# Optimization experiments

Hardware: AMD Instinct MI355X
Metric: run time of the kernel (lower is better)

The kernel has to match this reference:

```python
import jax, jax.numpy as jnp
import numpy as np

D_MODEL = 1024
HEADDIM = 64
EXPAND = 2
D_STATE = 128
D_CONV = 4
NGROUPS = 1
D_INNER = EXPAND * D_MODEL            # 2048
NHEADS = D_INNER // HEADDIM           # 32
CONV_DIM = D_INNER + 2 * NGROUPS * D_STATE
D_IN_PROJ = 2 * D_INNER + 2 * NGROUPS * D_STATE + NHEADS
BATCH = 2
SEQLEN = 1024
EPS = 1e-5


def silu(v):
    return v * jax.nn.sigmoid(v)


def setup_inputs() -> dict:
    key = jax.random.key(0)
    ks = jax.random.split(key, 8)
    s = 0.02
    return {
        "x": jax.random.normal(ks[0], (BATCH, SEQLEN, D_MODEL), jnp.float32),
        "in_proj_w": jax.random.normal(ks[1], (D_IN_PROJ, D_MODEL), jnp.float32) * s,
        "conv_w": jax.random.normal(ks[2], (CONV_DIM, D_CONV), jnp.float32) * 0.2,
        "conv_b": jax.random.normal(ks[3], (CONV_DIM,), jnp.float32) * 0.02,
        "dt_bias": jax.random.normal(ks[4], (NHEADS,), jnp.float32) * 0.1,
        "A_log": jax.random.normal(ks[5], (NHEADS,), jnp.float32) * 0.5,
        "D": jax.random.normal(ks[6], (NHEADS,), jnp.float32) * 0.5,
        "norm_w": jnp.ones((D_INNER,), jnp.float32),
        "out_proj_w": jax.random.normal(ks[7], (D_MODEL, D_INNER), jnp.float32) * s,
    }


def _mamba2(x, in_proj_w, conv_w, conv_b, dt_bias, A_log, D, norm_w, out_proj_w):
    b, l, _ = x.shape
    # input projection -> z | xBC | dt
    zxbcdt = x @ in_proj_w.T                                  # [b,l,d_in_proj]
    z, xBC, dt = jnp.split(zxbcdt, [D_INNER, D_INNER + CONV_DIM], axis=-1)
    dt = jax.nn.softplus(dt + dt_bias)                        # [b,l,nh]
    # causal depthwise conv over time, then SiLU
    rhs = conv_w.T[:, None, :]                                # [d_conv, 1, conv_dim]
    xBC = jax.lax.conv_general_dilated(
        xBC, rhs, window_strides=(1,), padding=[(D_CONV - 1, 0)],
        dimension_numbers=("NWC", "WIO", "NWC"), feature_group_count=CONV_DIM)
    xBC = silu(xBC + conv_b)
    xs, Bm, Cm = jnp.split(xBC, [D_INNER, D_INNER + D_STATE], axis=-1)
    xs = xs.reshape(b, l, NHEADS, HEADDIM)                    # [b,l,h,p]
    A = -jnp.exp(A_log)                                       # [nh], negative
    dA = jnp.exp(dt * A)                                      # [b,l,nh] in (0,1)
    # selective scan: h_t = dA_t * h_{t-1} + dt_t * x_t (outer) B_t; y_t = h_t C_t
    def step(h, inp):
        dA_t, x_t, B_t, dt_t, C_t = inp                       # [b,h],[b,h,p],[b,n],[b,h],[b,n]
        h = h * dA_t[:, :, None, None] + jnp.einsum("bh,bhp,bn->bhpn", dt_t, x_t, B_t)
        y = jnp.einsum("bhpn,bn->bhp", h, C_t)
        return h, y

    h0 = jnp.zeros((b, NHEADS, HEADDIM, D_STATE), x.dtype)
    xs_t = xs.transpose(1, 0, 2, 3)
    _, ys = jax.lax.scan(step, h0, (dA.transpose(1, 0, 2), xs_t,
                                    Bm.transpose(1, 0, 2), dt.transpose(1, 0, 2),
                                    Cm.transpose(1, 0, 2)))
    y = ys.transpose(1, 0, 2, 3) + D[None, None, :, None] * xs  # skip term
    y = y.reshape(b, l, D_INNER)
    # gated RMSNorm (norm_before_gate=False): rmsnorm(y * silu(z)) * w
    y = y * silu(z)
    y = y * jax.lax.rsqrt(jnp.mean(y * y, axis=-1, keepdims=True) + EPS) * norm_w
    return y @ out_proj_w.T


def reference(x, in_proj_w, conv_w, conv_b, dt_bias, A_log, D, norm_w, out_proj_w):
    return x + _mamba2(x, in_proj_w, conv_w, conv_b, dt_bias, A_log, D, norm_w, out_proj_w)
```

## Files before the change

kernel.cpp:

```cpp
#include <hip/hip_runtime.h>
#include <hip/hip_bf16.h>
#include <math.h>

#define NHEADS   32
#define CONV_DIM 2304
#define D_INNER  2048
#define SEQLEN   1024
#define NROWS    2048
#define ZX_STR   4352
#define D_MODEL  1024
#define Q        64
#define NCHUNK   16
#define XT_STR   72

typedef __attribute__((ext_vector_type(8))) short bhalf8;
typedef __attribute__((ext_vector_type(8))) short short8;
typedef __attribute__((ext_vector_type(4))) short short4v;
typedef __attribute__((ext_vector_type(4))) float f32x4;

__device__ __forceinline__ float bf2f(__hip_bfloat16 v){ return __bfloat162float(v); }
__device__ __forceinline__ short f2bs(float f){ __hip_bfloat16 h = __float2bfloat16(f); return *(short*)&h; }
__device__ __forceinline__ float s2f(short s){ __hip_bfloat16 h = *(__hip_bfloat16*)&s; return __bfloat162float(h); }
__device__ __forceinline__ float rdin(const void* p, size_t i, int isf){
    return isf ? ((const float*)p)[i] : __bfloat162float(((const __hip_bfloat16*)p)[i]);
}

__global__ __launch_bounds__(256)
void detect_dtype(const unsigned short* __restrict__ p, int* __restrict__ flag,
                  float* __restrict__ rowsum)
{
    for (int i = threadIdx.x; i < NROWS; i += 256) rowsum[i] = 0.f;
    int cnt = 0;
    for (int i = threadIdx.x; i < 4096; i += 256) {
        unsigned short u = p[2 * i];
        int e = (u >> 7) & 0xFF;
        cnt += (e >= 90 && e <= 141) ? 1 : 0;
    }
#pragma unroll
    for (int m = 1; m < 64; m <<= 1) cnt += __shfl_xor(cnt, m);
    __shared__ int red[4];
    if ((threadIdx.x & 63) == 0) red[threadIdx.x >> 6] = cnt;
    __syncthreads();
    if (threadIdx.x == 0) *flag = ((red[0]+red[1]+red[2]+red[3]) < 2048) ? 1 : 0;
}

#define XN8 262144
#define WN8 561152
#define ON8 262144
__global__ __launch_bounds__(256)
void to_bf16_all(const void* __restrict__ xs, const void* __restrict__ ws,
                 const void* __restrict__ os, const void* __restrict__ normw,
                 __hip_bfloat16* __restrict__ xd, __hip_bfloat16* __restrict__ wd,
                 __hip_bfloat16* __restrict__ od, const int* __restrict__ flagp)
{
    const int isf = *flagp;
    int i = blockIdx.x * 256 + threadIdx.x;
    if (i < XN8 + WN8) {
        const void* src; __hip_bfloat16* dst; int j;
        if (i < XN8) { src = xs; dst = xd; j = i; }
        else         { src = ws; dst = wd; j = i - XN8; }
        if (isf) {
            const float4* s = (const float4*)src;
            float4 a = s[2 * j], b = s[2 * j + 1];
            short8 r;
            r[0]=f2bs(a.x); r[1]=f2bs(a.y); r[2]=f2bs(a.z); r[3]=f2bs(a.w);
            r[4]=f2bs(b.x); r[5]=f2bs(b.y); r[6]=f2bs(b.z); r[7]=f2bs(b.w);
            ((short8*)dst)[j] = r;
        } else {
            ((float4*)dst)[j] = ((const float4*)src)[j];
        }
    } else {
        int j = i - XN8 - WN8;
        int k0 = (j * 8) & (D_INNER - 1);
        float v[8];
        if (isf) {
            const float4* s = (const float4*)os;
            float4 a = s[2 * j], b = s[2 * j + 1];
            v[0]=a.x; v[1]=a.y; v[2]=a.z; v[3]=a.w;
            v[4]=b.x; v[5]=b.y; v[6]=b.z; v[7]=b.w;
        } else {
            bhalf8 a = ((const bhalf8*)os)[j];
#pragma unroll
            for (int q = 0; q < 8; ++q) v[q] = s2f(a[q]);
        }
        short8 r;
#pragma unroll
        for (int q = 0; q < 8; ++q)
            r[q] = f2bs(v[q] * rdin(normw, k0 + q, isf));
        ((short8*)od)[j] = r;
    }
}

template<int MODE, int MT, int NT, int WROWS, int WCOLS>
__global__ __launch_bounds__(256)
void gemm_bt(const __hip_bfloat16* __restrict__ A,
             const __hip_bfloat16* __restrict__ W,
             __hip_bfloat16* __restrict__ Cb,
             const void* __restrict__ xraw,
             void* __restrict__ outv,
             const float* __restrict__ rowsum,
             const int* __restrict__ flagp,
             int K, int N)
{
    constexpr int FM = MT / WROWS / 16;
    constexpr int FN = NT / WCOLS / 16;
    constexpr int AI = MT / 32;
    constexpr int BI = NT / 32;
    __shared__ short As[MT * 64];
    __shared__ short Bs[NT * 64];
    const int m0 = blockIdx.y * MT;
    const int n0 = blockIdx.x * NT;
    const int wave = threadIdx.x >> 6;
    const int lane = threadIdx.x & 63;
    const int lr8 = lane >> 3, lc8 = lane & 7;
    const int lr  = lane & 15, lq  = lane >> 4;
    const int wm = (wave / WCOLS) * (MT / WROWS);
    const int wn = (wave % WCOLS) * (NT / WCOLS);
    const int swl = lr & 7;

    f32x4 acc[FM][FN];
#pragma unroll
    for (int i = 0; i < FM; ++i)
#pragma unroll
        for (int j = 0; j < FN; ++j) acc[i][j] = (f32x4){0.f,0.f,0.f,0.f};

    for (int k0 = 0; k0 < K; k0 += 64) {
#pragma unroll
        for (int i = 0; i < AI; ++i) {
            const int rt = (wave * AI + i) * 8;
            const __hip_bfloat16* gp = A + (size_t)(m0 + rt + lr8) * K + k0 + ((lc8 ^ lr8) << 3);
            __builtin_amdgcn_global_load_lds(
                (const __attribute__((address_space(1))) void*)gp,
                (__attribute__((address_space(3))) void*)&As[rt * 64], 16, 0, 0);
        }
#pragma unroll
        for (int i = 0; i < BI; ++i) {
            const int rt = (wave * BI + i) * 8;
            const __hip_bfloat16* gp = W + (size_t)(n0 + rt + lr8) * K + k0 + ((lc8 ^ lr8) << 3);
            __builtin_amdgcn_global_load_lds(
                (const __attribute__((address_space(1))) void*)gp,
                (__attribute__((address_space(3))) void*)&Bs[rt * 64], 16, 0, 0);
        }
        __syncthreads();
#pragma unroll
        for (int kk = 0; kk < 64; kk += 32) {
            const int sw = (((kk >> 3) + lq) ^ swl) << 3;
            bhalf8 af[FM], bfv[FN];
#pragma unroll
            for (int t = 0; t < FM; ++t)
                af[t]  = *(const bhalf8*)&As[(wm + t * 16 + lr) * 64 + sw];
#pragma unroll
            for (int t = 0; t < FN; ++t)
                bfv[t] = *(const bhalf8*)&Bs[(wn + t * 16 + lr) * 64 + sw];
#pragma unroll
            for (int ti = 0; ti < FM; ++ti)
#pragma unroll
                for (int tj = 0; tj < FN; ++tj)
                    acc[ti][tj] = __builtin_amdgcn_mfma_f32_16x16x32_bf16(
                        af[ti], bfv[tj], acc[ti][tj], 0, 0, 0);
        }
        __syncthreads();
    }

    const int isf = (MODE == 1) ? *flagp : 0;
#pragma unroll
    for (int ti = 0; ti < FM; ++ti)
#pragma unroll
        for (int tj = 0; tj < FN; ++tj)
#pragma unroll
            for (int r = 0; r < 4; ++r) {
                int m = m0 + wm + ti * 16 + lq * 4 + r;
                int n = n0 + wn + tj * 16 + lr;
                size_t idx = (size_t)m * N + n;
                float v = acc[ti][tj][r];
                if (MODE == 0) {
                    Cb[idx] = __float2bfloat16(v);
                } else {
                    float scale = rsqrtf(rowsum[m] / (float)D_INNER + 1e-5f);
                    v = v * scale + rdin(xraw, idx, isf);
                    if (isf) ((float*)outv)[idx] = v;
                    else     ((__hip_bfloat16*)outv)[idx] = __float2bfloat16(v);
                }
            }
}

__global__ __launch_bounds__(256)
void convdt(const __hip_bfloat16* __restrict__ zxb,
            const void* __restrict__ conv_w, const void* __restrict__ conv_b,
            const void* __restrict__ xraw, const void* __restrict__ wraw,
            const void* __restrict__ dt_bias,
            const int* __restrict__ flagp,
            __hip_bfloat16* __restrict__ xs_bf,
            __hip_bfloat16* __restrict__ B_bf,
            __hip_bfloat16* __restrict__ C_bf,
            float* __restrict__ dtp)
{
    __shared__ float xsh[8 * D_MODEL];
    const int isf = *flagp;

    if (blockIdx.x < 2304) {
        const int bx = blockIdx.x % 9, by = blockIdx.x / 9;
        const int seg = bx * 32 + (threadIdx.x & 31);
        const int c0 = seg * 8;
        const int row = by * 8 + (threadIdx.x >> 5);
        const int bstart = row & ~(SEQLEN - 1);
        bhalf8 in[4];
#pragma unroll
        for (int j = 0; j < 4; ++j) {
            int g = row - 3 + j;
            if (g >= bstart) {
                in[j] = *(const bhalf8*)&zxb[(size_t)g * ZX_STR + 2048 + c0];
            } else {
#pragma unroll
                for (int q = 0; q < 8; ++q) in[j][q] = 0;
            }
        }
        bhalf8 out;
#pragma unroll
        for (int j = 0; j < 8; ++j) {
            const int c = c0 + j;
            float acc = rdin(conv_b, c, isf);
            acc = fmaf(s2f(in[0][j]), rdin(conv_w, (size_t)c * 4 + 0, isf), acc);
            acc = fmaf(s2f(in[1][j]), rdin(conv_w, (size_t)c * 4 + 1, isf), acc);
            acc = fmaf(s2f(in[2][j]), rdin(conv_w, (size_t)c * 4 + 2, isf), acc);
            acc = fmaf(s2f(in[3][j]), rdin(conv_w, (size_t)c * 4 + 3, isf), acc);
            out[j] = f2bs(acc / (1.f + expf(-acc)));
        }
        if (c0 < 2048)      *(bhalf8*)&xs_bf[(size_t)row * 2048 + c0] = out;
        else if (c0 < 2176) *(bhalf8*)&B_bf[(size_t)row * 128 + (c0 - 2048)] = out;
        else                *(bhalf8*)&C_bf[(size_t)row * 128 + (c0 - 2176)] = out;
    } else {
        const int r0 = (blockIdx.x - 2304) * 8;
        if (isf) {
            const float4* xp = (const float4*)xraw;
            for (int i4 = threadIdx.x; i4 < 2048; i4 += 256)
                *(float4*)&xsh[i4 * 4] = xp[(size_t)r0 * 256 + i4];
        } else {
            const bhalf8* xp = (const bhalf8*)xraw;
            for (int i8 = threadIdx.x; i8 < 1024; i8 += 256) {
                bhalf8 v = xp[(size_t)r0 * 128 + i8];
#pragma unroll
                for (int q = 0; q < 8; ++q) xsh[i8 * 8 + q] = s2f(v[q]);
            }
        }
        __syncthreads();
        const int h = threadIdx.x >> 3;
        const int t = threadIdx.x & 7;
        const size_t wb = (size_t)(4352 + h) * D_MODEL;
        float s[8];
#pragma unroll
        for (int r = 0; r < 8; ++r) s[r] = 0.f;
        if (isf) {
            const float4* wp = (const float4*)wraw;
            for (int k0 = 0; k0 < D_MODEL; k0 += 32) {
                float4 w4 = wp[(wb + k0) / 4 + t];
#pragma unroll
                for (int r = 0; r < 8; ++r) {
                    float4 x4 = *(const float4*)&xsh[r * D_MODEL + k0 + t * 4];
                    s[r] = fmaf(w4.x, x4.x, fmaf(w4.y, x4.y,
                           fmaf(w4.z, x4.z, fmaf(w4.w, x4.w, s[r]))));
                }
            }
        } else {
            const __hip_bfloat16* wp = (const __hip_bfloat16*)wraw;
            for (int k0 = 0; k0 < D_MODEL; k0 += 64) {
                bhalf8 w8 = *(const bhalf8*)&wp[wb + k0 + t * 8];
#pragma unroll
                for (int r = 0; r < 8; ++r) {
                    float4 xa = *(const float4*)&xsh[r * D_MODEL + k0 + t * 8];
                    float4 xb = *(const float4*)&xsh[r * D_MODEL + k0 + t * 8 + 4];
                    s[r] = fmaf(s2f(w8[0]), xa.x, fmaf(s2f(w8[1]), xa.y,
                           fmaf(s2f(w8[2]), xa.z, fmaf(s2f(w8[3]), xa.w, s[r]))));
                    s[r] = fmaf(s2f(w8[4]), xb.x, fmaf(s2f(w8[5]), xb.y,
                           fmaf(s2f(w8[6]), xb.z, fmaf(s2f(w8[7]), xb.w, s[r]))));
                }
            }
        }
#pragma unroll
        for (int r = 0; r < 8; ++r) {
            s[r] += __shfl_xor(s[r], 1);
            s[r] += __shfl_xor(s[r], 2);
            s[r] += __shfl_xor(s[r], 4);
        }
        if (t == 0) {
            float bias = rdin(dt_bias, h, isf);
#pragma unroll
            for (int r = 0; r < 8; ++r) {
                float raw = s[r] + bias;
                dtp[(size_t)(r0 + r) * NHEADS + h] = raw > 20.f ? raw : log1pf(expf(raw));
            }
        }
    }
}

__global__ __launch_bounds__(256)
void chunk_kernel(const __hip_bfloat16* __restrict__ xs_bf,
                  const __hip_bfloat16* __restrict__ B_bf,
                  const __hip_bfloat16* __restrict__ C_bf,
                  const float* __restrict__ dtp, const void* __restrict__ Alog,
                  const int* __restrict__ flagp,
                  float* __restrict__ cumg, float* __restrict__ decayg,
                  __hip_bfloat16* __restrict__ M_bf,
                  __hip_bfloat16* __restrict__ Sb)
{
    __shared__ float cumS[Q], uS[Q], dtS[Q];
    __shared__ short Xt[64 * XT_STR];
    __shared__ short Bt[128 * XT_STR];
    const int bhc = blockIdx.x;
    const int c = bhc & 15, h = (bhc >> 4) & 31, b = bhc >> 9;
    const int row0 = b * SEQLEN + c * Q;
    const int isf = *flagp;

    if (threadIdx.x < 64) {
        const int t = threadIdx.x;
        const float An = -expf(rdin(Alog, h, isf));
        const float dt = dtp[(size_t)(row0 + t) * NHEADS + h];
        float cum = dt * An;
#pragma unroll
        for (int ofs = 1; ofs < 64; ofs <<= 1) {
            float v = __shfl_up(cum, ofs);
            if (t >= ofs) cum += v;
        }
        float tot = __shfl(cum, 63);
        cumS[t] = cum; dtS[t] = dt;
        uS[t] = expf(tot - cum) * dt;
        cumg[(size_t)bhc * Q + t] = cum;
        if (t == 63) decayg[bhc] = expf(tot);
    }
    __syncthreads();

#pragma unroll
    for (int i = 0; i < 2; ++i) {
        int seg = threadIdx.x + i * 256;
        int t = seg >> 3, p8 = (seg & 7) * 8;
        float ut = uS[t];
        bhalf8 v = *(const bhalf8*)&xs_bf[(size_t)(row0 + t) * 2048 + h * 64 + p8];
#pragma unroll
        for (int j = 0; j < 8; ++j)
            Xt[(p8 + j) * XT_STR + t] = f2bs(s2f(v[j]) * ut);
    }
#pragma unroll
    for (int i = 0; i < 4; ++i) {
        int seg = threadIdx.x + i * 256;
        int t = seg >> 4, n8 = (seg & 15) * 8;
        bhalf8 v = *(const bhalf8*)&B_bf[(size_t)(row0 + t) * 128 + n8];
#pragma unroll
        for (int j = 0; j < 8; ++j)
            Bt[(n8 + j) * XT_STR + t] = v[j];
    }

    const int wave = threadIdx.x >> 6, lane = threadIdx.x & 63;
    const int lr = lane & 15, lq = lane >> 4;

    {
        const int t0 = wave * 16;
        f32x4 acc[4];
#pragma unroll
        for (int j = 0; j < 4; ++j) acc[j] = (f32x4){0.f,0.f,0.f,0.f};
#pragma unroll
        for (int kk = 0; kk < 128; kk += 32) {
            bhalf8 af = *(const bhalf8*)&C_bf[(size_t)(row0 + t0 + lr) * 128 + kk + lq * 8];
#pragma unroll
            for (int j = 0; j < 4; ++j) {
                bhalf8 bf = *(const bhalf8*)&B_bf[(size_t)(row0 + j * 16 + lr) * 128 + kk + lq * 8];
                acc[j] = __builtin_amdgcn_mfma_f32_16x16x32_bf16(af, bf, acc[j], 0, 0, 0);
            }
        }
#pragma unroll
        for (int j = 0; j < 4; ++j)
#pragma unroll
            for (int r = 0; r < 4; ++r) {
                int t = t0 + lq * 4 + r;
                int s = j * 16 + lr;
                float m = (s <= t) ? acc[j][r] * expf(cumS[t] - cumS[s]) * dtS[s] : 0.f;
                M_bf[(size_t)bhc * 4096 + t * 64 + s] = __float2bfloat16(m);
            }
    }
    __syncthreads();

    {
        const int p0 = wave * 16;
        f32x4 acc[8];
#pragma unroll
        for (int j = 0; j < 8; ++j) acc[j] = (f32x4){0.f,0.f,0.f,0.f};
#pragma unroll
        for (int kk = 0; kk < 64; kk += 32) {
            bhalf8 af = *(const bhalf8*)&Xt[(p0 + lr) * XT_STR + kk + lq * 8];
#pragma unroll
            for (int j = 0; j < 8; ++j) {
                bhalf8 bf = *(const bhalf8*)&Bt[(j * 16 + lr) * XT_STR + kk + lq * 8];
                acc[j] = __builtin_amdgcn_mfma_f32_16x16x32_bf16(af, bf, acc[j], 0, 0, 0);
            }
        }
#pragma unroll
        for (int j = 0; j < 8; ++j)
#pragma unroll
            for (int r = 0; r < 4; ++r) {
                int p = p0 + lq * 4 + r;
                int n = j * 16 + lr;
                Sb[(size_t)bhc * 8192 + p * 128 + n] = __float2bfloat16(acc[j][r]);
            }
    }
}

__global__ __launch_bounds__(256)
void rec_kernel(const __hip_bfloat16* __restrict__ Sb,
                const float* __restrict__ decayg,
                __hip_bfloat16* __restrict__ hst)
{
    const int bh = blockIdx.x >> 3;
    const int sl = blockIdx.x & 7;
    const int off = sl * 1024 + threadIdx.x * 4;
    float h0 = 0.f, h1 = 0.f, h2 = 0.f, h3 = 0.f;
    for (int c = 0; c < NCHUNK; ++c) {
        size_t base = ((size_t)bh * NCHUNK + c) * 8192 + off;
        short4v hb;
        hb[0] = f2bs(h0); hb[1] = f2bs(h1); hb[2] = f2bs(h2); hb[3] = f2bs(h3);
        *(short4v*)&hst[base] = hb;
        short4v sv = *(const short4v*)&Sb[base];
        float d = decayg[bh * NCHUNK + c];
        h0 = fmaf(h0, d, s2f(sv[0])); h1 = fmaf(h1, d, s2f(sv[1]));
        h2 = fmaf(h2, d, s2f(sv[2])); h3 = fmaf(h3, d, s2f(sv[3]));
    }
}

__global__ __launch_bounds__(256)
void y_kernel(const __hip_bfloat16* __restrict__ M_bf,
              const __hip_bfloat16* __restrict__ xs_bf,
              const __hip_bfloat16* __restrict__ C_bf,
              const __hip_bfloat16* __restrict__ hst,
              const float* __restrict__ cumg,
              const __hip_bfloat16* __restrict__ zxb,
              const void* __restrict__ Draw, const int* __restrict__ flagp,
              __hip_bfloat16* __restrict__ vbuf, float* __restrict__ rowsum)
{
    __shared__ short Xt[64 * XT_STR];
    __shared__ short zS[64 * XT_STR];
    const int bhc = blockIdx.x;
    const int c = bhc & 15, h = (bhc >> 4) & 31, b = bhc >> 9;
    const int row0 = b * SEQLEN + c * Q;
    const int isf = *flagp;
    const float Dh = rdin(Draw, h, isf);

#pragma unroll
    for (int i = 0; i < 2; ++i) {
        int seg = threadIdx.x + i * 256;
        int t = seg >> 3, p8 = (seg & 7) * 8;
        bhalf8 v = *(const bhalf8*)&xs_bf[(size_t)(row0 + t) * 2048 + h * 64 + p8];
#pragma unroll
        for (int j = 0; j < 8; ++j)
            Xt[(p8 + j) * XT_STR + t] = v[j];
        bhalf8 zv = *(const bhalf8*)&zxb[(size_t)(row0 + t) * ZX_STR + h * 64 + p8];
        *(bhalf8*)&zS[t * XT_STR + p8] = zv;
    }
    __syncthreads();

    const int wave = threadIdx.x >> 6, lane = threadIdx.x & 63;
    const int lr = lane & 15, lq = lane >> 4;
    const int t0 = wave * 16;
    f32x4 acc1[4], acc2[4];
#pragma unroll
    for (int j = 0; j < 4; ++j) { acc1[j] = (f32x4){0.f,0.f,0.f,0.f}; acc2[j] = acc1[j]; }

#pragma unroll
    for (int kk = 0; kk < 64; kk += 32) {
        bhalf8 af = *(const bhalf8*)&M_bf[(size_t)bhc * 4096 + (t0 + lr) * 64 + kk + lq * 8];
#pragma unroll
        for (int j = 0; j < 4; ++j) {
            bhalf8 bf = *(const bhalf8*)&Xt[(j * 16 + lr) * XT_STR + kk + lq * 8];
            acc1[j] = __builtin_amdgcn_mfma_f32_16x16x32_bf16(af, bf, acc1[j], 0, 0, 0);
        }
    }
#pragma unroll
    for (int kk = 0; kk < 128; kk += 32) {
        bhalf8 af = *(const bhalf8*)&C_bf[(size_t)(row0 + t0 + lr) * 128 + kk + lq * 8];
#pragma unroll
        for (int j = 0; j < 4; ++j) {
            bhalf8 bf = *(const bhalf8*)&hst[(size_t)bhc * 8192 + (j * 16 + lr) * 128 + kk + lq * 8];
            acc2[j] = __builtin_amdgcn_mfma_f32_16x16x32_bf16(af, bf, acc2[j], 0, 0, 0);
        }
    }
    float ex[4];
#pragma unroll
    for (int r = 0; r < 4; ++r) ex[r] = expf(cumg[(size_t)bhc * Q + t0 + lq * 4 + r]);

    float vv[4][4];
    float s2[4] = {0.f, 0.f, 0.f, 0.f};
#pragma unroll
    for (int j = 0; j < 4; ++j)
#pragma unroll
        for (int r = 0; r < 4; ++r) {
            int t = t0 + lq * 4 + r;
            int p = j * 16 + lr;
            float xv = s2f(Xt[p * XT_STR + t]);
            float y = acc1[j][r] + ex[r] * acc2[j][r] + Dh * xv;
            float zz = s2f(zS[t * XT_STR + p]);
            float v = y * (zz / (1.f + expf(-zz)));
            vv[j][r] = v;
            s2[r] += v * v;
        }
#pragma unroll
    for (int r = 0; r < 4; ++r) {
        s2[r] += __shfl_xor(s2[r], 1);
        s2[r] += __shfl_xor(s2[r], 2);
        s2[r] += __shfl_xor(s2[r], 4);
        s2[r] += __shfl_xor(s2[r], 8);
    }
    if (lr == 0)
#pragma unroll
        for (int r = 0; r < 4; ++r)
            atomicAdd(&rowsum[row0 + t0 + lq * 4 + r], s2[r]);

    __syncthreads();
#pragma unroll
    for (int j = 0; j < 4; ++j)
#pragma unroll
        for (int r = 0; r < 4; ++r)
            zS[(t0 + lq * 4 + r) * XT_STR + j * 16 + lr] = f2bs(vv[j][r]);
    __syncthreads();
#pragma unroll
    for (int i = 0; i < 2; ++i) {
        int seg = threadIdx.x + i * 256;
        int t = seg >> 3, p8 = (seg & 7) * 8;
        bhalf8 o = *(const bhalf8*)&zS[t * XT_STR + p8];
        *(bhalf8*)&vbuf[(size_t)(row0 + t) * D_INNER + h * 64 + p8] = o;
    }
}

extern "C" void kernel_launch(void* const* d_in, const int* in_sizes, int n_in,
                              void* d_out, int out_size, void* d_ws, size_t ws_size,
                              hipStream_t stream)
{
    const void* x_raw    = d_in[0];
    const void* inw_raw  = d_in[1];
    const void* convw    = d_in[2];
    const void* convb    = d_in[3];
    const void* dtb      = d_in[4];
    const void* Alog     = d_in[5];
    const void* Dsk      = d_in[6];
    const void* normw    = d_in[7];
    const void* outw_raw = d_in[8];

    char* ws = (char*)d_ws;
    size_t off = 0;
    int* flag = (int*)(ws + off);                      off += 256;
    float* rowsum = (float*)(ws + off);                off += (size_t)NROWS * 4;
    __hip_bfloat16* xb    = (__hip_bfloat16*)(ws+off); off += (size_t)NROWS * D_MODEL * 2;
    __hip_bfloat16* inwb  = (__hip_bfloat16*)(ws+off); off += (size_t)4384 * D_MODEL * 2;
    __hip_bfloat16* outwb = (__hip_bfloat16*)(ws+off); off += (size_t)D_MODEL * D_INNER * 2;
    __hip_bfloat16* zxb   = (__hip_bfloat16*)(ws+off); off += (size_t)NROWS * ZX_STR * 2;
    __hip_bfloat16* xs_bf = (__hip_bfloat16*)(ws+off); off += (size_t)NROWS * 2048 * 2;
    __hip_bfloat16* B_bf  = (__hip_bfloat16*)(ws+off); off += (size_t)NROWS * 128 * 2;
    __hip_bfloat16* C_bf  = (__hip_bfloat16*)(ws+off); off += (size_t)NROWS * 128 * 2;
    float* dtp   = (float*)(ws+off);                   off += (size_t)NROWS * NHEADS * 4;
    float* cumg  = (float*)(ws+off);                   off += (size_t)1024 * Q * 4;
    float* decayg= (float*)(ws+off);                   off += (size_t)1024 * 4;
    __hip_bfloat16* M_bf  = (__hip_bfloat16*)(ws+off); off += (size_t)1024 * 4096 * 2;
    __hip_bfloat16* hst   = (__hip_bfloat16*)(ws+off); off += (size_t)1024 * 8192 * 2;
    __hip_bfloat16* Sb    = (__hip_bfloat16*)(ws+off); off += (size_t)1024 * 8192 * 2;
    __hip_bfloat16* vbuf = Sb;

    detect_dtype<<<1, 256, 0, stream>>>((const unsigned short*)x_raw, flag, rowsum);
    to_bf16_all<<<(XN8+WN8+ON8)/256, 256, 0, stream>>>(x_raw, inw_raw, outw_raw,
                                                       normw, xb, inwb, outwb, flag);
    gemm_bt<0,64,128,1,4><<<dim3(34, 32), 256, 0, stream>>>(
        xb, inwb, zxb, nullptr, nullptr, nullptr, flag, D_MODEL, ZX_STR);
    convdt<<<2560, 256, 0, stream>>>(zxb, convw, convb, x_raw, inw_raw, dtb, flag,
                                     xs_bf, B_bf, C_bf, dtp);
    chunk_kernel<<<1024, 256, 0, stream>>>(xs_bf, B_bf, C_bf, dtp, Alog, flag,
                                           cumg, decayg, M_bf, Sb);
    rec_kernel<<<512, 256, 0, stream>>>(Sb, decayg, hst);
    y_kernel<<<1024, 256, 0, stream>>>(M_bf, xs_bf, C_bf, hst, cumg, zxb, Dsk,
                                       flag, vbuf, rowsum);
    gemm_bt<1,64,64,2,2><<<dim3(16, 32), 256, 0, stream>>>(
        vbuf, outwb, nullptr, x_raw, d_out, rowsum, flag, D_INNER, D_MODEL);
}
```

Measured before the change: 270.8 us.

## Stage conv input rows in LDS and reuse across 8 output rows

The depthwise conv part of convdt now has each block load 11 rows (8 outputs plus the 3-row halo) of all conv channels into shared memory once. Each thread then loads conv weights and bias vectorised into registers and computes 8 consecutive rows, instead of reloading 4 input rows and scalar weights per output. This cuts redundant global reads of zxb and conv_w and shrinks the grid from 2304 to 256 conv blocks. In exchange each block does more serial work, occupancy may drop because shared memory grows to about 50KB, and the dt part of the kernel now reuses that buffer.

```diff
diff --git a/kernel.cpp b/kernel.cpp
--- a/kernel.cpp
+++ b/kernel.cpp
@@ -195,42 +195,87 @@
             __hip_bfloat16* __restrict__ C_bf,
             float* __restrict__ dtp)
 {
-    __shared__ float xsh[8 * D_MODEL];
+    __shared__ short smem[11 * CONV_DIM];
     const int isf = *flagp;
 
-    if (blockIdx.x < 2304) {
-        const int bx = blockIdx.x % 9, by = blockIdx.x / 9;
-        const int seg = bx * 32 + (threadIdx.x & 31);
-        const int c0 = seg * 8;
-        const int row = by * 8 + (threadIdx.x >> 5);
-        const int bstart = row & ~(SEQLEN - 1);
-        bhalf8 in[4];
-#pragma unroll
-        for (int j = 0; j < 4; ++j) {
-            int g = row - 3 + j;
+    if (blockIdx.x < 256) {
+        const int r0 = blockIdx.x * 8;
+        const int bstart = r0 & ~(SEQLEN - 1);
+        for (int idx = threadIdx.x; idx < 11 * (CONV_DIM / 8); idx += 256) {
+            int ii = idx / (CONV_DIM / 8);
+            int seg = idx % (CONV_DIM / 8);
+            int g = r0 - 3 + ii;
+            bhalf8 v;
             if (g >= bstart) {
-                in[j] = *(const bhalf8*)&zxb[(size_t)g * ZX_STR + 2048 + c0];
+                v = *(const bhalf8*)&zxb[(size_t)g * ZX_STR + 2048 + seg * 8];
             } else {
 #pragma unroll
-                for (int q = 0; q < 8; ++q) in[j][q] = 0;
-            }
-        }
-        bhalf8 out;
-#pragma unroll
-        for (int j = 0; j < 8; ++j) {
-            const int c = c0 + j;
-            float acc = rdin(conv_b, c, isf);
-            acc = fmaf(s2f(in[0][j]), rdin(conv_w, (size_t)c * 4 + 0, isf), acc);
-            acc = fmaf(s2f(in[1][j]), rdin(conv_w, (size_t)c * 4 + 1, isf), acc);
-            acc = fmaf(s2f(in[2][j]), rdin(conv_w, (size_t)c * 4 + 2, isf), acc);
-            acc = fmaf(s2f(in[3][j]), rdin(conv_w, (size_t)c * 4 + 3, isf), acc);
-            out[j] = f2bs(acc / (1.f + expf(-acc)));
-        }
-        if (c0 < 2048)      *(bhalf8*)&xs_bf[(size_t)row * 2048 + c0] = out;
-        else if (c0 < 2176) *(bhalf8*)&B_bf[(size_t)row * 128 + (c0 - 2048)] = out;
-        else                *(bhalf8*)&C_bf[(size_t)row * 128 + (c0 - 2176)] = out;
+                for (int j = 0; j < 8; ++j) v[j] = 0;
+            }
+            *(bhalf8*)&smem[ii * CONV_DIM + seg * 8] = v;
+        }
+        __syncthreads();
+
+#pragma unroll
+        for (int sIt = 0; sIt < 2; ++sIt) {
+            const int seg = threadIdx.x + sIt * 256;
+            if (seg >= CONV_DIM / 8) break;
+            const int c0 = seg * 8;
+            float wt[8][4], bias[8];
+            if (isf) {
+                const float4* wp = (const float4*)conv_w;
+#pragma unroll
+                for (int u = 0; u < 8; ++u) {
+                    float4 q = wp[c0 + u];
+                    wt[u][0]=q.x; wt[u][1]=q.y; wt[u][2]=q.z; wt[u][3]=q.w;
+                }
+                float4 b0 = ((const float4*)conv_b)[seg * 2];
+                float4 b1 = ((const float4*)conv_b)[seg * 2 + 1];
+                bias[0]=b0.x; bias[1]=b0.y; bias[2]=b0.z; bias[3]=b0.w;
+                bias[4]=b1.x; bias[5]=b1.y; bias[6]=b1.z; bias[7]=b1.w;
+            } else {
+                const bhalf8* wp = (const bhalf8*)conv_w;
+#pragma unroll
+                for (int u = 0; u < 4; ++u) {
+                    bhalf8 q = wp[seg * 4 + u];
+#pragma unroll
+                    for (int t4 = 0; t4 < 4; ++t4) {
+                        wt[2*u][t4]   = s2f(q[t4]);
+                        wt[2*u+1][t4] = s2f(q[4 + t4]);
+                    }
+                }
+                bhalf8 bq = ((const bhalf8*)conv_b)[seg];
+#pragma unroll
+                for (int j = 0; j < 8; ++j) bias[j] = s2f(bq[j]);
+            }
+#pragma unroll
+            for (int r = 0; r < 8; ++r) {
+                bhalf8 i0 = *(const bhalf8*)&smem[(r + 0) * CONV_DIM + c0];
+                bhalf8 i1 = *(const bhalf8*)&smem[(r + 1) * CONV_DIM + c0];
+                bhalf8 i2 = *(const bhalf8*)&smem[(r + 2) * CONV_DIM + c0];
+                bhalf8 i3 = *(const bhalf8*)&smem[(r + 3) * CONV_DIM + c0];
+                bhalf8 out;
+#pragma unroll
+                for (int j = 0; j < 8; ++j) {
+                    float acc = bias[j];
+                    acc = fmaf(s2f(i0[j]), wt[j][0], acc);
+                    acc = fmaf(s2f(i1[j]), wt[j][1], acc);
+                    acc = fmaf(s2f(i2[j]), wt[j][2], acc);
+                    acc = fmaf(s2f(i3[j]), wt[j][3], acc);
+                    out[j] = f2bs(acc / (1.f + expf(-acc)));
+                }
+                const int row = r0 + r;
+                if (c0 < 2048)
+                    *(bhalf8*)&xs_bf[(size_t)row * 2048 + c0] = out;
+                else if (c0 < 2176)
+                    *(bhalf8*)&B_bf[(size_t)row * 128 + (c0 - 2048)] = out;
+                else
+                    *(bhalf8*)&C_bf[(size_t)row * 128 + (c0 - 2176)] = out;
+            }
+        }
     } else {
-        const int r0 = (blockIdx.x - 2304) * 8;
+        float* xsh = (float*)smem;
+        const int r0 = (blockIdx.x - 256) * 8;
         if (isf) {
             const float4* xp = (const float4*)xraw;
             for (int i4 = threadIdx.x; i4 < 2048; i4 += 256)
@@ -565,8 +610,8 @@
                                                        normw, xb, inwb, outwb, flag);
     gemm_bt<0,64,128,1,4><<<dim3(34, 32), 256, 0, stream>>>(
         xb, inwb, zxb, nullptr, nullptr, nullptr, flag, D_MODEL, ZX_STR);
-    convdt<<<2560, 256, 0, stream>>>(zxb, convw, convb, x_raw, inw_raw, dtb, flag,
-                                     xs_bf, B_bf, C_bf, dtp);
+    convdt<<<512, 256, 0, stream>>>(zxb, convw, convb, x_raw, inw_raw, dtb, flag,
+                                    xs_bf, B_bf, C_bf, dtp);
     chunk_kernel<<<1024, 256, 0, stream>>>(xs_bf, B_bf, C_bf, dtp, Alog, flag,
                                            cumg, decayg, M_bf, Sb);
     rec_kernel<<<512, 256, 0, stream>>>(Sb, decayg, hst);
```

Result: faster. 224.6 us (-17.1%).
